# Optimization experiments

Measured on AMD Instinct MI355X. Metric: run time of the kernel, lower is better.

## Reference

```python
import jax, jax.numpy as jnp
import numpy as np
from jax import lax

D_MODEL = 1024
D_STATE = 16
D_CONV = 4
EXPAND = 2
D_INNER = EXPAND * D_MODEL  # 2048
DT_RANK = (D_MODEL + 15) // 16  # 64 (ceil(d_model/16), mamba default)
BATCH = 2
SEQLEN = 1024


def setup_inputs() -> dict:
    key = jax.random.key(0)
    ks = jax.random.split(key, 12)
    s = lambda k, shape, sc=0.02: jax.random.normal(k, shape, jnp.float32) * sc
    # A init: S4D-real, A_log = log(1..d_state) tiled over channels
    A_log = jnp.log(jnp.tile(jnp.arange(1, D_STATE + 1, dtype=jnp.float32), (D_INNER, 1)))
    # dt bias init so softplus(dt_bias) ~ 0.01
    dt_bias = jnp.log(jnp.expm1(jnp.full((D_INNER,), 0.01, jnp.float32)))
    return {
        "x": jax.random.normal(ks[0], (BATCH, SEQLEN, D_MODEL), jnp.float32),
        "in_proj_w": s(ks[1], (2 * D_INNER, D_MODEL)),
        "conv_w": s(ks[2], (D_INNER, 1, D_CONV), 0.1),
        "conv_b": s(ks[3], (D_INNER,), 0.1),
        "x_proj_w": s(ks[4], (DT_RANK + 2 * D_STATE, D_INNER)),
        "dt_proj_w": s(ks[5], (D_INNER, DT_RANK), 0.1),
        "dt_proj_b": dt_bias,
        "A_log": A_log,
        "D": jnp.ones((D_INNER,), jnp.float32),
        "out_proj_w": s(ks[6], (D_MODEL, D_INNER)),
        "ln1_g": jnp.ones((D_MODEL,), jnp.float32),
        "ln1_b": jnp.zeros((D_MODEL,), jnp.float32),
        "ln2_g": jnp.ones((D_MODEL,), jnp.float32),
        "ln2_b": jnp.zeros((D_MODEL,), jnp.float32),
        "ffn_w1": s(ks[7], (4 * D_MODEL, D_MODEL)),
        "ffn_b1": jnp.zeros((4 * D_MODEL,), jnp.float32),
        "ffn_w2": s(ks[8], (D_MODEL, 4 * D_MODEL)),
        "ffn_b2": jnp.zeros((D_MODEL,), jnp.float32),
    }


def _layernorm(x, g, b, eps=1e-5):
    mu = jnp.mean(x, axis=-1, keepdims=True)
    var = jnp.mean(jnp.square(x - mu), axis=-1, keepdims=True)
    return (x - mu) * lax.rsqrt(var + eps) * g + b


def _mamba(x, in_proj_w, conv_w, conv_b, x_proj_w, dt_proj_w, dt_proj_b,
           A_log, D, out_proj_w):
    Bsz, L, _ = x.shape
    xz = x @ in_proj_w.T                       # [B, L, 2*d_inner]
    xi, z = jnp.split(xz, 2, axis=-1)          # each [B, L, d_inner]
    # causal depthwise conv1d over time
    xc = xi.transpose(0, 2, 1)                 # [B, d_inner, L]
    xc = lax.conv_general_dilated(
        xc, conv_w, window_strides=(1,), padding=[(D_CONV - 1, 0)],
        feature_group_count=D_INNER,
        dimension_numbers=("NCH", "OIH", "NCH"))
    xc = xc + conv_b[None, :, None]
    xc = jax.nn.silu(xc).transpose(0, 2, 1)    # [B, L, d_inner]
    # input-dependent SSM params
    x_dbl = xc @ x_proj_w.T                    # [B, L, dt_rank + 2*d_state]
    dt, Bmat, Cmat = jnp.split(x_dbl, [DT_RANK, DT_RANK + D_STATE], axis=-1)
    dt = jax.nn.softplus(dt @ dt_proj_w.T + dt_proj_b)   # [B, L, d_inner]
    A = -jnp.exp(A_log)                        # [d_inner, d_state]
    dA = jnp.exp(dt[..., None] * A)                       # [B, L, d_inner, d_state]
    dBx = dt[..., None] * Bmat[:, :, None, :] * xc[..., None]  # [B, L, d_inner, d_state]
    # selective scan over time
    def step(h, inp):
        dA_t, dBx_t, C_t = inp
        h = dA_t * h + dBx_t                   # [B, d_inner, d_state]
        y = jnp.einsum("bdn,bn->bd", h, C_t)
        return h, y
    h0 = jnp.zeros((Bsz, D_INNER, D_STATE), x.dtype)
    _, ys = lax.scan(step, h0,
                     (dA.transpose(1, 0, 2, 3),
                      dBx.transpose(1, 0, 2, 3),
                      Cmat.transpose(1, 0, 2)))
    y = ys.transpose(1, 0, 2)                  # [B, L, d_inner]
    y = y + D * xc
    y = y * jax.nn.silu(z)
    return y @ out_proj_w.T                    # [B, L, d_model]


def reference(x, in_proj_w, conv_w, conv_b, x_proj_w, dt_proj_w, dt_proj_b,
              A_log, D, out_proj_w, ln1_g, ln1_b, ln2_g, ln2_b,
              ffn_w1, ffn_b1, ffn_w2, ffn_b2):
    # x = x + Mamba(LN1(x))
    x = x + _mamba(_layernorm(x, ln1_g, ln1_b), in_proj_w, conv_w, conv_b,
                   x_proj_w, dt_proj_w, dt_proj_b, A_log, D, out_proj_w)
    # x = x + FFN(LN2(x))  (dropout inactive in eval)
    h = _layernorm(x, ln2_g, ln2_b)
    f = jax.nn.relu(h @ ffn_w1.T + ffn_b1) @ ffn_w2.T + ffn_b2
    return x + f
```

## Files before the change

kernel.cpp:

```cpp
#include <hip/hip_runtime.h>
#include <hip/hip_bf16.h>

#define T_TOK 2048
#define LSEQ  1024
#define DM    1024
#define DI    2048
#define LDW2  72

using bf16 = __hip_bfloat16;
typedef __attribute__((ext_vector_type(8))) short short8;
typedef __attribute__((ext_vector_type(4))) float floatx4;

__device__ inline float to_f(float v) { return v; }
__device__ inline float to_f(bf16 v) { return __bfloat162float(v); }
__device__ inline bf16  f2bf(float v) { return __float2bfloat16(v); }
__device__ inline float bf2f(short s) { return __bfloat162float(__builtin_bit_cast(bf16, s)); }

__device__ inline short8 ld8(const bf16* p) { return *(const short8*)p; }
__device__ inline short8 ld8(const float* p) {
    floatx4 f0 = *(const floatx4*)p;
    floatx4 f1 = *(const floatx4*)(p + 4);
    short8 r;
#pragma unroll
    for (int i = 0; i < 4; ++i) {
        r[i]     = __builtin_bit_cast(short, __float2bfloat16(f0[i]));
        r[i + 4] = __builtin_bit_cast(short, __float2bfloat16(f1[i]));
    }
    return r;
}

__device__ __forceinline__ void gload16(const void* g, void* l) {
    __builtin_amdgcn_global_load_lds(
        (const __attribute__((address_space(1))) unsigned int*)g,
        (__attribute__((address_space(3))) unsigned int*)l, 16, 0, 0);
}

__device__ __forceinline__ int swz32(int row, int col) {
    return row * 32 + (col ^ (((row >> 1) & 3) << 3));
}

template<int EPI, int KS>
__device__ __forceinline__ void gemm_core(
    const bf16* __restrict__ A, int lda,
    const bf16* __restrict__ W, int K,
    float* __restrict__ outF, bf16* __restrict__ outB, int ldc,
    const float* __restrict__ bias, size_t zstr)
{
    __shared__ __align__(16) bf16 sA[128 * 32];
    __shared__ __align__(16) bf16 sW[128 * 32];
    const int tid  = threadIdx.x;
    const int lane = tid & 63, wid = tid >> 6;

    const int nwg = gridDim.x * gridDim.y * gridDim.z;
    const int lin = blockIdx.x + gridDim.x * (blockIdx.y + gridDim.y * blockIdx.z);
    const int sid = (lin & 7) * (nwg >> 3) + (lin >> 3);
    const int bx  = sid % gridDim.x;
    const int byz = sid / gridDim.x;
    const int by  = byz % gridDim.y;
    const int bz  = byz / gridDim.y;

    const int m0 = bx * 128, n0 = by * 128;
    const int wm = (wid >> 1) * 64, wn = (wid & 1) * 64;
    const int lr = lane & 15, lh = lane >> 4;

    const int r0  = tid >> 2;
    const int gc0 = ((tid & 3) * 8) ^ (((r0 >> 1) & 3) << 3);

    const int kBeg = bz * (K / KS);
    const int kEnd = kBeg + K / KS;

    const bf16* Ag0 = A + (size_t)(m0 + r0)      * lda + kBeg + gc0;
    const bf16* Ag1 = A + (size_t)(m0 + r0 + 64) * lda + kBeg + gc0;
    const bf16* Wg0 = W + (size_t)(n0 + r0)      * K   + kBeg + gc0;
    const bf16* Wg1 = W + (size_t)(n0 + r0 + 64) * K   + kBeg + gc0;

    bf16* sA0 = sA + wid * 512;
    bf16* sA1 = sA + 2048 + wid * 512;
    bf16* sW0 = sW + wid * 512;
    bf16* sW1 = sW + 2048 + wid * 512;

    floatx4 acc[4][4];
#pragma unroll
    for (int i = 0; i < 4; ++i)
#pragma unroll
        for (int j = 0; j < 4; ++j) acc[i][j] = (floatx4){0.f, 0.f, 0.f, 0.f};

    for (int k0 = kBeg; k0 < kEnd; k0 += 32) {
        __syncthreads();
        gload16(Ag0, sA0);
        gload16(Ag1, sA1);
        gload16(Wg0, sW0);
        gload16(Wg1, sW1);
        Ag0 += 32; Ag1 += 32; Wg0 += 32; Wg1 += 32;
        __syncthreads();

        short8 af[4], wf[4];
#pragma unroll
        for (int i = 0; i < 4; ++i)
            af[i] = *(const short8*)(sA + swz32(wm + i * 16 + lr, lh * 8));
#pragma unroll
        for (int j = 0; j < 4; ++j)
            wf[j] = *(const short8*)(sW + swz32(wn + j * 16 + lr, lh * 8));
#pragma unroll
        for (int i = 0; i < 4; ++i)
#pragma unroll
            for (int j = 0; j < 4; ++j)
                acc[i][j] = __builtin_amdgcn_mfma_f32_16x16x32_bf16(af[i], wf[j], acc[i][j], 0, 0, 0);
    }

#pragma unroll
    for (int i = 0; i < 4; ++i) {
#pragma unroll
        for (int j = 0; j < 4; ++j) {
#pragma unroll
            for (int r = 0; r < 4; ++r) {
                int row = m0 + wm + i * 16 + lh * 4 + r;
                int col = n0 + wn + j * 16 + lr;
                size_t off = (size_t)row * ldc + col;
                float c = acc[i][j][r];
                if (EPI == 0) {
                    outB[off] = f2bf(c);
                } else if (EPI == 2) {
                    float v = c + bias[col];
                    outB[off] = f2bf((v > 15.f) ? v : log1pf(__expf(v)));
                } else if (EPI == 4) {
                    float v = c + bias[col];
                    outB[off] = f2bf(v > 0.f ? v : 0.f);
                } else if (EPI == 7) {
                    outF[off + (size_t)bz * zstr] = c;
                } else if (EPI == 8) {
                    outB[off + (size_t)bz * zstr] = f2bf(c);
                }
            }
        }
    }
}

__launch_bounds__(256, 3)
__global__ void g_inproj(const bf16* __restrict__ A, const bf16* __restrict__ W,
                         bf16* __restrict__ outB)
{ gemm_core<0, 1>(A, DM, W, DM, nullptr, outB, 4096, nullptr, 0); }

__launch_bounds__(256, 3)
__global__ void g_xproj(const bf16* __restrict__ A, const bf16* __restrict__ W,
                        float* __restrict__ outF)
{ gemm_core<7, 16>(A, DI, W, DI, outF, nullptr, 128, nullptr, (size_t)T_TOK * 128); }

__launch_bounds__(256, 3)
__global__ void g_outproj(const bf16* __restrict__ A, const bf16* __restrict__ W,
                          bf16* __restrict__ outB)
{ gemm_core<8, 4>(A, DI, W, DI, nullptr, outB, DM, nullptr, (size_t)T_TOK * DM); }

__launch_bounds__(256, 3)
__global__ void g_ffn1(const bf16* __restrict__ A, const bf16* __restrict__ W,
                       bf16* __restrict__ outB, const float* __restrict__ bias)
{ gemm_core<4, 1>(A, DM, W, DM, nullptr, outB, 4096, bias, 0); }

__launch_bounds__(256, 3)
__global__ void g_ffn2_4(const bf16* __restrict__ A, const bf16* __restrict__ W,
                         bf16* __restrict__ outB)
{ gemm_core<8, 4>(A, 4096, W, 4096, nullptr, outB, DM, nullptr, (size_t)T_TOK * DM); }

__launch_bounds__(256, 3)
__global__ void g_ffn2_2(const bf16* __restrict__ A, const bf16* __restrict__ W,
                         bf16* __restrict__ outB)
{ gemm_core<8, 2>(A, 4096, W, 4096, nullptr, outB, DM, nullptr, (size_t)T_TOK * DM); }

__launch_bounds__(256)
__global__ void cvtw(const float* __restrict__ src, bf16* __restrict__ dst)
{
    size_t i = ((size_t)blockIdx.x * 256 + threadIdx.x) * 8;
    *(short8*)(dst + i) = ld8(src + i);
}

__launch_bounds__(256)
__global__ void cvtw4(const float* __restrict__ s0, bf16* __restrict__ d0,
                      const float* __restrict__ s1, bf16* __restrict__ d1,
                      const float* __restrict__ s2, bf16* __restrict__ d2,
                      const float* __restrict__ s3, bf16* __restrict__ d3)
{
    constexpr size_t N0 = (size_t)2 * DI * DM;
    constexpr size_t N1 = (size_t)DM * DI;
    constexpr size_t N2 = (size_t)4 * DM * DM;
    size_t i = ((size_t)blockIdx.x * 256 + threadIdx.x) * 8;
    if (i < N0) { *(short8*)(d0 + i) = ld8(s0 + i); return; }
    i -= N0;
    if (i < N1) { *(short8*)(d1 + i) = ld8(s1 + i); return; }
    i -= N1;
    if (i < N2) { *(short8*)(d2 + i) = ld8(s2 + i); return; }
    i -= N2;
    *(short8*)(d3 + i) = ld8(s3 + i);
}

__launch_bounds__(256)
__global__ void gemm_dt64(const float* __restrict__ A,
                          const float* __restrict__ W,
                          const float* __restrict__ bias,
                          bf16* __restrict__ outB)
{
    __shared__ __align__(16) bf16 sA[32 * LDW2];
    __shared__ __align__(16) bf16 sW[128 * LDW2];
    const int tid = threadIdx.x;
    const int lane = tid & 63, w = tid >> 6;
    const int m0 = blockIdx.x * 32, n0 = blockIdx.y * 128;

    {
        int ar = tid >> 3, ac = (tid & 7) * 8;
        *(short8*)(sA + ar * LDW2 + ac) = ld8(A + (size_t)(m0 + ar) * 128 + ac);
        int wr = tid >> 1, wc = (tid & 1) * 32;
        const float* wp = W + (size_t)(n0 + wr) * 64 + wc;
        *(short8*)(sW + wr * LDW2 + wc)      = ld8(wp);
        *(short8*)(sW + wr * LDW2 + wc + 8)  = ld8(wp + 8);
        *(short8*)(sW + wr * LDW2 + wc + 16) = ld8(wp + 16);
        *(short8*)(sW + wr * LDW2 + wc + 24) = ld8(wp + 24);
    }
    __syncthreads();

    const int lr = lane & 15, lh = lane >> 4;
    floatx4 acc[2][2];
#pragma unroll
    for (int i = 0; i < 2; ++i)
#pragma unroll
        for (int j = 0; j < 2; ++j) acc[i][j] = (floatx4){0.f, 0.f, 0.f, 0.f};

#pragma unroll
    for (int kk = 0; kk < 2; ++kk) {
        short8 af[2], wf[2];
#pragma unroll
        for (int i = 0; i < 2; ++i)
            af[i] = *(const short8*)(sA + (i * 16 + lr) * LDW2 + kk * 32 + lh * 8);
#pragma unroll
        for (int j = 0; j < 2; ++j)
            wf[j] = *(const short8*)(sW + (w * 32 + j * 16 + lr) * LDW2 + kk * 32 + lh * 8);
#pragma unroll
        for (int i = 0; i < 2; ++i)
#pragma unroll
            for (int j = 0; j < 2; ++j)
                acc[i][j] = __builtin_amdgcn_mfma_f32_16x16x32_bf16(af[i], wf[j], acc[i][j], 0, 0, 0);
    }

#pragma unroll
    for (int i = 0; i < 2; ++i) {
#pragma unroll
        for (int j = 0; j < 2; ++j) {
#pragma unroll
            for (int r = 0; r < 4; ++r) {
                int row = m0 + i * 16 + lh * 4 + r;
                int col = n0 + w * 32 + j * 16 + lr;
                float v = acc[i][j][r] + bias[col];
                outB[(size_t)row * DI + col] = f2bf((v > 15.f) ? v : log1pf(__expf(v)));
            }
        }
    }
}

__launch_bounds__(256)
__global__ void reduce16(const float* __restrict__ P, float* __restrict__ out)
{
    int i = blockIdx.x * 256 + threadIdx.x;
    const floatx4* P4 = (const floatx4*)P;
    floatx4 s = (floatx4){0.f, 0.f, 0.f, 0.f};
#pragma unroll
    for (int z = 0; z < 16; ++z) s += P4[(size_t)z * 65536 + i];
    ((floatx4*)out)[i] = s;
}

__launch_bounds__(256)
__global__ void red4_resid(const bf16* __restrict__ P, const float* __restrict__ x,
                           float* __restrict__ out)
{
    size_t base = ((size_t)blockIdx.x * 256 + threadIdx.x) * 8;
    floatx4 x0 = *(const floatx4*)(x + base);
    floatx4 x1 = *(const floatx4*)(x + base + 4);
    float s[8];
#pragma unroll
    for (int j = 0; j < 4; ++j) { s[j] = x0[j]; s[j + 4] = x1[j]; }
#pragma unroll
    for (int z = 0; z < 4; ++z) {
        short8 p = *(const short8*)(P + (size_t)z * T_TOK * DM + base);
#pragma unroll
        for (int j = 0; j < 8; ++j) s[j] += bf2f(p[j]);
    }
    *(floatx4*)(out + base)     = (floatx4){s[0], s[1], s[2], s[3]};
    *(floatx4*)(out + base + 4) = (floatx4){s[4], s[5], s[6], s[7]};
}

template<int Z>
__launch_bounds__(256)
__global__ void red_bias_resid(const bf16* __restrict__ P, const float* __restrict__ bias,
                               const float* __restrict__ resid, float* __restrict__ out)
{
    size_t base = ((size_t)blockIdx.x * 256 + threadIdx.x) * 8;
    int c = (int)(base & (DM - 1));
    floatx4 b0 = *(const floatx4*)(bias + c);
    floatx4 b1 = *(const floatx4*)(bias + c + 4);
    floatx4 x0 = *(const floatx4*)(resid + base);
    floatx4 x1 = *(const floatx4*)(resid + base + 4);
    float s[8];
#pragma unroll
    for (int j = 0; j < 4; ++j) { s[j] = x0[j] + b0[j]; s[j + 4] = x1[j] + b1[j]; }
#pragma unroll
    for (int z = 0; z < Z; ++z) {
        short8 p = *(const short8*)(P + (size_t)z * T_TOK * DM + base);
#pragma unroll
        for (int j = 0; j < 8; ++j) s[j] += bf2f(p[j]);
    }
    *(floatx4*)(out + base)     = (floatx4){s[0], s[1], s[2], s[3]};
    *(floatx4*)(out + base + 4) = (floatx4){s[4], s[5], s[6], s[7]};
}

__launch_bounds__(256)
__global__ void ln_kernel(const float* __restrict__ x, const float* __restrict__ g,
                          const float* __restrict__ bb, bf16* __restrict__ out)
{
    int t = blockIdx.x, tid = threadIdx.x;
    const float* xr = x + (size_t)t * DM;
    float v[4], s = 0.f, ss = 0.f;
#pragma unroll
    for (int i = 0; i < 4; ++i) {
        v[i] = xr[tid + i * 256];
        s += v[i]; ss += v[i] * v[i];
    }
#pragma unroll
    for (int o = 1; o < 64; o <<= 1) { s += __shfl_xor(s, o); ss += __shfl_xor(ss, o); }
    __shared__ float red[8];
    int lane = tid & 63, wid = tid >> 6;
    if (lane == 0) { red[wid] = s; red[wid + 4] = ss; }
    __syncthreads();
    s  = red[0] + red[1] + red[2] + red[3];
    ss = red[4] + red[5] + red[6] + red[7];
    float mu  = s * (1.f / DM);
    float var = ss * (1.f / DM) - mu * mu;
    float rs  = rsqrtf(var + 1e-5f);
#pragma unroll
    for (int i = 0; i < 4; ++i) {
        int c = tid + i * 256;
        out[(size_t)t * DM + c] = f2bf((v[i] - mu) * rs * g[c] + bb[c]);
    }
}

__launch_bounds__(256)
__global__ void conv_silu(const bf16* __restrict__ xz, const float* __restrict__ cw,
                          const float* __restrict__ cb, bf16* __restrict__ xcb)
{
    int idx = (blockIdx.x * 256 + threadIdx.x) * 8;
    int d  = idx & (DI - 1);
    int tk = idx >> 11;
    int t  = tk & (LSEQ - 1);
    const short8 zero = {0, 0, 0, 0, 0, 0, 0, 0};
    short8 x3 = ld8(xz + (size_t)tk * 4096 + d);
    short8 x2 = (t >= 1) ? ld8(xz + (size_t)(tk - 1) * 4096 + d) : zero;
    short8 x1 = (t >= 2) ? ld8(xz + (size_t)(tk - 2) * 4096 + d) : zero;
    short8 x0 = (t >= 3) ? ld8(xz + (size_t)(tk - 3) * 4096 + d) : zero;
    short8 r;
#pragma unroll
    for (int j = 0; j < 8; ++j) {
        floatx4 wv = *(const floatx4*)(cw + (size_t)(d + j) * 4);
        float acc = cb[d + j]
                  + wv[0] * bf2f(x0[j]) + wv[1] * bf2f(x1[j])
                  + wv[2] * bf2f(x2[j]) + wv[3] * bf2f(x3[j]);
        float s = acc / (1.f + __expf(-acc));
        r[j] = __builtin_bit_cast(short, f2bf(s));
    }
    *(short8*)(xcb + idx) = r;
}

__launch_bounds__(256)
__global__ void padw_kernel(const float* __restrict__ w, bf16* __restrict__ wp)
{
    int idx = blockIdx.x * 256 + threadIdx.x;
    int row = idx >> 11;
    wp[idx] = (row < 96) ? f2bf(w[idx]) : f2bf(0.f);
}

template<int NCH_>
__launch_bounds__(256)
__global__ void scan_part1(const bf16* __restrict__ dt, const bf16* __restrict__ xc,
                           const float* __restrict__ xdbl, const float* __restrict__ A_log,
                           float* __restrict__ Ssum, float* __restrict__ hend)
{
    constexpr int CLEN_ = LSEQ / NCH_;
    constexpr int LOGN  = (NCH_ == 64) ? 6 : 5;
    int G = blockIdx.x * 256 + threadIdx.x;
    int half = G & 1;
    int d = (G >> 1) & (DI - 1);
    int c = (G >> 12) & (NCH_ - 1);
    int b = G >> (12 + LOGN);
    int n0 = half * 8;

    floatx4 al0 = *(const floatx4*)(A_log + d * 16 + n0);
    floatx4 al1 = *(const floatx4*)(A_log + d * 16 + n0 + 4);
    float a[8];
#pragma unroll
    for (int j = 0; j < 4; ++j) { a[j] = -__expf(al0[j]); a[j + 4] = -__expf(al1[j]); }

    const bf16*  dt_p = dt   + (size_t)b * LSEQ * DI + d;
    const bf16*  xc_p = xc   + (size_t)b * LSEQ * DI + d;
    const float* xb_p = xdbl + (size_t)b * LSEQ * 128 + 64 + n0;

    float h[8];
#pragma unroll
    for (int j = 0; j < 8; ++j) h[j] = 0.f;
    float S = 0.f;

    const int t0 = c * CLEN_;
#pragma unroll 4
    for (int t = t0; t < t0 + CLEN_; ++t) {
        float dtv = to_f(dt_p[(size_t)t * DI]);
        float xv  = to_f(xc_p[(size_t)t * DI]);
        floatx4 B0 = *(const floatx4*)(xb_p + (size_t)t * 128);
        floatx4 B1 = *(const floatx4*)(xb_p + (size_t)t * 128 + 4);
        S += dtv;
        float dx = dtv * xv;
#pragma unroll
        for (int j = 0; j < 4; ++j) {
            h[j]     = fmaf(__expf(dtv * a[j]),     h[j],     dx * B0[j]);
            h[j + 4] = fmaf(__expf(dtv * a[j + 4]), h[j + 4], dx * B1[j]);
        }
    }

    size_t cid = (size_t)(b * NCH_ + c) * DI + d;
    if (half == 0) Ssum[cid] = S;
    float* he = hend + cid * 16 + n0;
    *(floatx4*)he       = (floatx4){h[0], h[1], h[2], h[3]};
    *(floatx4*)(he + 4) = (floatx4){h[4], h[5], h[6], h[7]};
}

template<int NCH_>
__launch_bounds__(256)
__global__ void scan_prefix(const float* __restrict__ A_log, const float* __restrict__ Ssum,
                            float* __restrict__ hend)
{
    int tid = blockIdx.x * 256 + threadIdx.x;
    int n = tid & 15;
    int d = (tid >> 4) & (DI - 1);
    int b = tid >> 15;
    float a = -__expf(A_log[d * 16 + n]);

    size_t row = (size_t)b * NCH_ * DI + d;
    float Sc = Ssum[row];
    float E  = hend[row * 16 + n];
    float h = 0.f;
    for (int c = 0; c < NCH_; ++c) {
        size_t nrow = row + DI;
        float Sn = 0.f, En = 0.f;
        if (c + 1 < NCH_) { Sn = Ssum[nrow]; En = hend[nrow * 16 + n]; }
        float P = __expf(a * Sc);
        hend[row * 16 + n] = h;
        h  = fmaf(P, h, E);
        Sc = Sn; E = En; row = nrow;
    }
}

template<int NCH_>
__launch_bounds__(256)
__global__ void scan_part2(const bf16* __restrict__ dt, const bf16* __restrict__ xc,
                           const float* __restrict__ xdbl, const bf16* __restrict__ xz,
                           const float* __restrict__ hinit, const float* __restrict__ A_log,
                           const float* __restrict__ Dp, bf16* __restrict__ Y)
{
    constexpr int CLEN_ = LSEQ / NCH_;
    constexpr int LOGN  = (NCH_ == 64) ? 6 : 5;
    int G = blockIdx.x * 256 + threadIdx.x;
    int half = G & 1;
    int d = (G >> 1) & (DI - 1);
    int c = (G >> 12) & (NCH_ - 1);
    int b = G >> (12 + LOGN);
    int n0 = half * 8;

    floatx4 al0 = *(const floatx4*)(A_log + d * 16 + n0);
    floatx4 al1 = *(const floatx4*)(A_log + d * 16 + n0 + 4);
    float a[8];
#pragma unroll
    for (int j = 0; j < 4; ++j) { a[j] = -__expf(al0[j]); a[j + 4] = -__expf(al1[j]); }
    float Dd = Dp[d];

    size_t cid = (size_t)(b * NCH_ + c) * DI + d;
    const float* hi = hinit + cid * 16 + n0;
    floatx4 h0 = *(const floatx4*)hi;
    floatx4 h1 = *(const floatx4*)(hi + 4);
    float h[8] = {h0[0], h0[1], h0[2], h0[3], h1[0], h1[1], h1[2], h1[3]};

    const bf16*  dt_p = dt   + (size_t)b * LSEQ * DI + d;
    const bf16*  xc_p = xc   + (size_t)b * LSEQ * DI + d;
    const float* xb_p = xdbl + (size_t)b * LSEQ * 128 + 64 + n0;
    const float* xcc_p= xdbl + (size_t)b * LSEQ * 128 + 80 + n0;
    const bf16*  z_p  = xz   + (size_t)b * LSEQ * 4096 + DI + d;
    bf16* y_p = Y + (size_t)b * LSEQ * DI + d;

    const int t0 = c * CLEN_;
#pragma unroll 4
    for (int t = t0; t < t0 + CLEN_; ++t) {
        float dtv = to_f(dt_p[(size_t)t * DI]);
        float xv  = to_f(xc_p[(size_t)t * DI]);
        float zv  = to_f(z_p[(size_t)t * 4096]);
        floatx4 B0 = *(const floatx4*)(xb_p  + (size_t)t * 128);
        floatx4 B1 = *(const floatx4*)(xb_p  + (size_t)t * 128 + 4);
        floatx4 C0 = *(const floatx4*)(xcc_p + (size_t)t * 128);
        floatx4 C1 = *(const floatx4*)(xcc_p + (size_t)t * 128 + 4);
        float dx = dtv * xv;
        float p = 0.f;
#pragma unroll
        for (int j = 0; j < 4; ++j) {
            h[j]     = fmaf(__expf(dtv * a[j]),     h[j],     dx * B0[j]);
            p = fmaf(h[j], C0[j], p);
            h[j + 4] = fmaf(__expf(dtv * a[j + 4]), h[j + 4], dx * B1[j]);
            p = fmaf(h[j + 4], C1[j], p);
        }
        p += __shfl_xor(p, 1);
        if (half == 0) {
            float pp = p + Dd * xv;
            float sz = zv / (1.f + __expf(-zv));
            y_p[(size_t)t * DI] = f2bf(pp * sz);
        }
    }
}

extern "C" void kernel_launch(void* const* d_in, const int* in_sizes, int n_in,
                              void* d_out, int out_size, void* d_ws, size_t ws_size,
                              hipStream_t stream)
{
    const float* x       = (const float*)d_in[0];
    const float* in_proj = (const float*)d_in[1];
    const float* conv_w  = (const float*)d_in[2];
    const float* conv_b  = (const float*)d_in[3];
    const float* x_proj  = (const float*)d_in[4];
    const float* dt_w    = (const float*)d_in[5];
    const float* dt_b    = (const float*)d_in[6];
    const float* A_log   = (const float*)d_in[7];
    const float* Dp      = (const float*)d_in[8];
    const float* out_w   = (const float*)d_in[9];
    const float* ln1g    = (const float*)d_in[10];
    const float* ln1b    = (const float*)d_in[11];
    const float* ln2g    = (const float*)d_in[12];
    const float* ln2b    = (const float*)d_in[13];
    const float* fw1     = (const float*)d_in[14];
    const float* fb1     = (const float*)d_in[15];
    const float* fw2     = (const float*)d_in[16];
    const float* fb2     = (const float*)d_in[17];
    float* out = (float*)d_out;

    char* w = (char*)d_ws;
    bf16*  h1   = (bf16*)(w);
    bf16*  xz   = (bf16*)(w + (4u  << 20));
    bf16*  xc   = (bf16*)(w + (20u << 20));
    float* xdf  = (float*)(w + (28u << 20));
    bf16*  dtb  = (bf16*)(w + (29u << 20));
    float* Pp   = (float*)(w + (29u << 20));
    float* hend = (float*)(w + (37u << 20));
    float* x2   = (float*)(w + (37u << 20));
    bf16*  Wpad = (bf16*)(w + (45u << 20));
    float* Ssum = (float*)(w);
    bf16*  Pout = (bf16*)(w + (4u  << 20));
    bf16*  Yb = xc;
    bf16*  f1 = xz;

    const bool roomy = ws_size >= ((size_t)74 << 20);

    if (roomy) {
        bf16* ipB  = (bf16*)(w + (46u << 20));
        bf16* owB  = (bf16*)(w + (54u << 20));
        bf16* fw1B = (bf16*)(w + (58u << 20));
        bf16* fw2B = (bf16*)(w + (66u << 20));
        bf16* Pf   = (bf16*)(w + (20u << 20));

        cvtw4<<<dim3(7168), dim3(256), 0, stream>>>(in_proj, ipB, out_w, owB,
                                                    fw1, fw1B, fw2, fw2B);
        ln_kernel<<<dim3(T_TOK), dim3(256), 0, stream>>>(x, ln1g, ln1b, h1);
        g_inproj<<<dim3(16, 32), dim3(256), 0, stream>>>(h1, ipB, xz);
        conv_silu<<<dim3(T_TOK * DI / 8 / 256), dim3(256), 0, stream>>>(xz, conv_w, conv_b, xc);
        padw_kernel<<<dim3(128 * 2048 / 256), dim3(256), 0, stream>>>(x_proj, Wpad);
        g_xproj<<<dim3(16, 1, 16), dim3(256), 0, stream>>>(xc, Wpad, Pp);
        reduce16<<<dim3(256), dim3(256), 0, stream>>>(Pp, xdf);
        gemm_dt64<<<dim3(64, 16), dim3(256), 0, stream>>>(xdf, dt_w, dt_b, dtb);
        scan_part1<64><<<dim3(2048), dim3(256), 0, stream>>>(dtb, xc, xdf, A_log, Ssum, hend);
        scan_prefix<64><<<dim3(256), dim3(256), 0, stream>>>(A_log, Ssum, hend);
        scan_part2<64><<<dim3(2048), dim3(256), 0, stream>>>(dtb, xc, xdf, xz, hend, A_log, Dp, Yb);
        g_outproj<<<dim3(16, 8, 4), dim3(256), 0, stream>>>(Yb, owB, Pout);
        red4_resid<<<dim3(1024), dim3(256), 0, stream>>>(Pout, x, x2);
        ln_kernel<<<dim3(T_TOK), dim3(256), 0, stream>>>(x2, ln2g, ln2b, h1);
        g_ffn1<<<dim3(16, 32), dim3(256), 0, stream>>>(h1, fw1B, f1, fb1);
        g_ffn2_4<<<dim3(16, 8, 4), dim3(256), 0, stream>>>(f1, fw2B, Pf);
        red_bias_resid<4><<<dim3(1024), dim3(256), 0, stream>>>(Pf, fb2, x2, out);
    } else {
        bf16* ipB  = (bf16*)(w + (20u << 20));
        bf16* owB  = (bf16*)(w);
        bf16* fw1B = (bf16*)(w + (29u << 20));
        bf16* fw2B = (bf16*)(w + (20u << 20));
        bf16* Pf   = (bf16*)(w + (28u << 20));

        cvtw<<<dim3(2048), dim3(256), 0, stream>>>(in_proj, ipB);
        ln_kernel<<<dim3(T_TOK), dim3(256), 0, stream>>>(x, ln1g, ln1b, h1);
        g_inproj<<<dim3(16, 32), dim3(256), 0, stream>>>(h1, ipB, xz);
        conv_silu<<<dim3(T_TOK * DI / 8 / 256), dim3(256), 0, stream>>>(xz, conv_w, conv_b, xc);
        padw_kernel<<<dim3(128 * 2048 / 256), dim3(256), 0, stream>>>(x_proj, Wpad);
        g_xproj<<<dim3(16, 1, 16), dim3(256), 0, stream>>>(xc, Wpad, Pp);
        reduce16<<<dim3(256), dim3(256), 0, stream>>>(Pp, xdf);
        gemm_dt64<<<dim3(64, 16), dim3(256), 0, stream>>>(xdf, dt_w, dt_b, dtb);
        scan_part1<32><<<dim3(1024), dim3(256), 0, stream>>>(dtb, xc, xdf, A_log, Ssum, hend);
        scan_prefix<32><<<dim3(256), dim3(256), 0, stream>>>(A_log, Ssum, hend);
        cvtw<<<dim3(1024), dim3(256), 0, stream>>>(out_w, owB);
        scan_part2<32><<<dim3(1024), dim3(256), 0, stream>>>(dtb, xc, xdf, xz, hend, A_log, Dp, Yb);
        g_outproj<<<dim3(16, 8, 4), dim3(256), 0, stream>>>(Yb, owB, Pout);
        red4_resid<<<dim3(1024), dim3(256), 0, stream>>>(Pout, x, x2);
        cvtw<<<dim3(2048), dim3(256), 0, stream>>>(fw1, fw1B);
        ln_kernel<<<dim3(T_TOK), dim3(256), 0, stream>>>(x2, ln2g, ln2b, h1);
        g_ffn1<<<dim3(16, 32), dim3(256), 0, stream>>>(h1, fw1B, f1, fb1);
        cvtw<<<dim3(2048), dim3(256), 0, stream>>>(fw2, fw2B);
        g_ffn2_2<<<dim3(16, 8, 2), dim3(256), 0, stream>>>(f1, fw2B, Pf);
        red_bias_resid<2><<<dim3(1024), dim3(256), 0, stream>>>(Pf, fb2, x2, out);
    }
}
```

Baseline: 357.7 us.

## Double-buffer GEMM LDS tiles, fuse residual reduce with LN2, fold x_proj padding into weight conversion

The shared GEMM core now keeps two LDS stages and issues the next tile's global-to-LDS loads before the MFMA work on the current tile, so memory latency overlaps compute and there is one barrier per k-step instead of two. The split-K residual reduction is merged with the second layernorm into a single per-token kernel, which removes one launch and one reread of x2. The x_proj padding is folded into the batched weight-conversion kernel, removing another launch. The costs are double the LDS per block, which may lower occupancy under launch_bounds(256,3), and an extra dummy load of a wrapped-around tile on the last iteration.

```diff
diff --git a/kernel.cpp b/kernel.cpp
--- a/kernel.cpp
+++ b/kernel.cpp
@@ -9,6 +9,7 @@
 
 using bf16 = __hip_bfloat16;
 typedef __attribute__((ext_vector_type(8))) short short8;
+typedef __attribute__((ext_vector_type(4))) short short4b;
 typedef __attribute__((ext_vector_type(4))) float floatx4;
 
 __device__ inline float to_f(float v) { return v; }
@@ -46,8 +47,8 @@
     float* __restrict__ outF, bf16* __restrict__ outB, int ldc,
     const float* __restrict__ bias, size_t zstr)
 {
-    __shared__ __align__(16) bf16 sA[128 * 32];
-    __shared__ __align__(16) bf16 sW[128 * 32];
+    __shared__ __align__(16) bf16 sA[2][128 * 32];
+    __shared__ __align__(16) bf16 sW[2][128 * 32];
     const int tid  = threadIdx.x;
     const int lane = tid & 63, wid = tid >> 6;
 
@@ -69,15 +70,10 @@
     const int kBeg = bz * (K / KS);
     const int kEnd = kBeg + K / KS;
 
-    const bf16* Ag0 = A + (size_t)(m0 + r0)      * lda + kBeg + gc0;
-    const bf16* Ag1 = A + (size_t)(m0 + r0 + 64) * lda + kBeg + gc0;
-    const bf16* Wg0 = W + (size_t)(n0 + r0)      * K   + kBeg + gc0;
-    const bf16* Wg1 = W + (size_t)(n0 + r0 + 64) * K   + kBeg + gc0;
-
-    bf16* sA0 = sA + wid * 512;
-    bf16* sA1 = sA + 2048 + wid * 512;
-    bf16* sW0 = sW + wid * 512;
-    bf16* sW1 = sW + 2048 + wid * 512;
+    const bf16* aR0 = A + (size_t)(m0 + r0)      * lda + gc0;
+    const bf16* aR1 = A + (size_t)(m0 + r0 + 64) * lda + gc0;
+    const bf16* wR0 = W + (size_t)(n0 + r0)      * K   + gc0;
+    const bf16* wR1 = W + (size_t)(n0 + r0 + 64) * K   + gc0;
 
     floatx4 acc[4][4];
 #pragma unroll
@@ -85,28 +81,51 @@
 #pragma unroll
         for (int j = 0; j < 4; ++j) acc[i][j] = (floatx4){0.f, 0.f, 0.f, 0.f};
 
-    for (int k0 = kBeg; k0 < kEnd; k0 += 32) {
-        __syncthreads();
-        gload16(Ag0, sA0);
-        gload16(Ag1, sA1);
-        gload16(Wg0, sW0);
-        gload16(Wg1, sW1);
-        Ag0 += 32; Ag1 += 32; Wg0 += 32; Wg1 += 32;
-        __syncthreads();
-
-        short8 af[4], wf[4];
-#pragma unroll
-        for (int i = 0; i < 4; ++i)
-            af[i] = *(const short8*)(sA + swz32(wm + i * 16 + lr, lh * 8));
-#pragma unroll
-        for (int j = 0; j < 4; ++j)
-            wf[j] = *(const short8*)(sW + swz32(wn + j * 16 + lr, lh * 8));
-#pragma unroll
-        for (int i = 0; i < 4; ++i)
-#pragma unroll
-            for (int j = 0; j < 4; ++j)
-                acc[i][j] = __builtin_amdgcn_mfma_f32_16x16x32_bf16(af[i], wf[j], acc[i][j], 0, 0, 0);
-    }
+#define STAGE(B, KK) do {                                       \
+        gload16(aR0 + (KK), &sA[B][wid * 512]);                 \
+        gload16(aR1 + (KK), &sA[B][2048 + wid * 512]);          \
+        gload16(wR0 + (KK), &sW[B][wid * 512]);                 \
+        gload16(wR1 + (KK), &sW[B][2048 + wid * 512]);          \
+    } while (0)
+
+#define COMPUTE(B) do {                                                        \
+        short8 af[4], wf[4];                                                   \
+        _Pragma("unroll")                                                      \
+        for (int i = 0; i < 4; ++i)                                            \
+            af[i] = *(const short8*)(&sA[B][swz32(wm + i * 16 + lr, lh * 8)]); \
+        _Pragma("unroll")                                                      \
+        for (int j = 0; j < 4; ++j)                                            \
+            wf[j] = *(const short8*)(&sW[B][swz32(wn + j * 16 + lr, lh * 8)]); \
+        _Pragma("unroll")                                                      \
+        for (int i = 0; i < 4; ++i)                                            \
+            _Pragma("unroll")                                                  \
+            for (int j = 0; j < 4; ++j)                                        \
+                acc[i][j] = __builtin_amdgcn_mfma_f32_16x16x32_bf16(           \
+                    af[i], wf[j], acc[i][j], 0, 0, 0);                         \
+    } while (0)
+
+#define PHASE_SYNC() do {                                       \
+        __builtin_amdgcn_sched_barrier(0);                      \
+        asm volatile("s_waitcnt vmcnt(0)" ::: "memory");        \
+        __builtin_amdgcn_s_barrier();                           \
+        __builtin_amdgcn_sched_barrier(0);                      \
+    } while (0)
+
+    STAGE(0, kBeg);
+    PHASE_SYNC();
+
+    for (int k0 = kBeg; k0 < kEnd; k0 += 64) {
+        STAGE(1, k0 + 32);
+        COMPUTE(0);
+        PHASE_SYNC();
+        int kn = (k0 + 64 < kEnd) ? k0 + 64 : kBeg;
+        STAGE(0, kn);
+        COMPUTE(1);
+        PHASE_SYNC();
+    }
+#undef STAGE
+#undef COMPUTE
+#undef PHASE_SYNC
 
 #pragma unroll
     for (int i = 0; i < 4; ++i) {
@@ -174,14 +193,16 @@
 }
 
 __launch_bounds__(256)
-__global__ void cvtw4(const float* __restrict__ s0, bf16* __restrict__ d0,
+__global__ void cvtw5(const float* __restrict__ s0, bf16* __restrict__ d0,
                       const float* __restrict__ s1, bf16* __restrict__ d1,
                       const float* __restrict__ s2, bf16* __restrict__ d2,
-                      const float* __restrict__ s3, bf16* __restrict__ d3)
+                      const float* __restrict__ s3, bf16* __restrict__ d3,
+                      const float* __restrict__ s4, bf16* __restrict__ d4)
 {
     constexpr size_t N0 = (size_t)2 * DI * DM;
     constexpr size_t N1 = (size_t)DM * DI;
     constexpr size_t N2 = (size_t)4 * DM * DM;
+    constexpr size_t N3 = (size_t)DM * 4 * DM;
     size_t i = ((size_t)blockIdx.x * 256 + threadIdx.x) * 8;
     if (i < N0) { *(short8*)(d0 + i) = ld8(s0 + i); return; }
     i -= N0;
@@ -189,7 +210,11 @@
     i -= N1;
     if (i < N2) { *(short8*)(d2 + i) = ld8(s2 + i); return; }
     i -= N2;
-    *(short8*)(d3 + i) = ld8(s3 + i);
+    if (i < N3) { *(short8*)(d3 + i) = ld8(s3 + i); return; }
+    i -= N3;
+    int row = (int)(i >> 11);
+    if (row < 96) { *(short8*)(d4 + i) = ld8(s4 + i); }
+    else { *(short8*)(d4 + i) = (short8){0,0,0,0,0,0,0,0}; }
 }
 
 __launch_bounds__(256)
@@ -266,23 +291,42 @@
 }
 
 __launch_bounds__(256)
-__global__ void red4_resid(const bf16* __restrict__ P, const float* __restrict__ x,
-                           float* __restrict__ out)
-{
-    size_t base = ((size_t)blockIdx.x * 256 + threadIdx.x) * 8;
-    floatx4 x0 = *(const floatx4*)(x + base);
-    floatx4 x1 = *(const floatx4*)(x + base + 4);
-    float s[8];
-#pragma unroll
-    for (int j = 0; j < 4; ++j) { s[j] = x0[j]; s[j + 4] = x1[j]; }
+__global__ void red4_ln(const bf16* __restrict__ P, const float* __restrict__ x,
+                        const float* __restrict__ g, const float* __restrict__ bb,
+                        float* __restrict__ x2, bf16* __restrict__ h1)
+{
+    int t = blockIdx.x, tid = threadIdx.x;
+    size_t rowoff = (size_t)t * DM + tid * 4;
+    floatx4 xv = *(const floatx4*)(x + rowoff);
+    float v[4];
+#pragma unroll
+    for (int i = 0; i < 4; ++i) v[i] = xv[i];
 #pragma unroll
     for (int z = 0; z < 4; ++z) {
-        short8 p = *(const short8*)(P + (size_t)z * T_TOK * DM + base);
-#pragma unroll
-        for (int j = 0; j < 8; ++j) s[j] += bf2f(p[j]);
-    }
-    *(floatx4*)(out + base)     = (floatx4){s[0], s[1], s[2], s[3]};
-    *(floatx4*)(out + base + 4) = (floatx4){s[4], s[5], s[6], s[7]};
+        short4b p = *(const short4b*)(P + (size_t)z * T_TOK * DM + rowoff);
+#pragma unroll
+        for (int i = 0; i < 4; ++i) v[i] += bf2f(p[i]);
+    }
+    *(floatx4*)(x2 + rowoff) = (floatx4){v[0], v[1], v[2], v[3]};
+    float s = v[0] + v[1] + v[2] + v[3];
+    float ss = v[0]*v[0] + v[1]*v[1] + v[2]*v[2] + v[3]*v[3];
+#pragma unroll
+    for (int o = 1; o < 64; o <<= 1) { s += __shfl_xor(s, o); ss += __shfl_xor(ss, o); }
+    __shared__ float red[8];
+    int lane = tid & 63, wid = tid >> 6;
+    if (lane == 0) { red[wid] = s; red[wid + 4] = ss; }
+    __syncthreads();
+    s  = red[0] + red[1] + red[2] + red[3];
+    ss = red[4] + red[5] + red[6] + red[7];
+    float mu  = s * (1.f / DM);
+    float var = ss * (1.f / DM) - mu * mu;
+    float rs  = rsqrtf(var + 1e-5f);
+    int c = tid * 4;
+    short4b o4;
+#pragma unroll
+    for (int i = 0; i < 4; ++i)
+        o4[i] = __builtin_bit_cast(short, f2bf((v[i] - mu) * rs * g[c + i] + bb[c + i]));
+    *(short4b*)(h1 + rowoff) = o4;
 }
 
 template<int Z>
@@ -564,12 +608,11 @@
         bf16* fw2B = (bf16*)(w + (66u << 20));
         bf16* Pf   = (bf16*)(w + (20u << 20));
 
-        cvtw4<<<dim3(7168), dim3(256), 0, stream>>>(in_proj, ipB, out_w, owB,
-                                                    fw1, fw1B, fw2, fw2B);
+        cvtw5<<<dim3(7296), dim3(256), 0, stream>>>(in_proj, ipB, out_w, owB,
+                                                    fw1, fw1B, fw2, fw2B, x_proj, Wpad);
         ln_kernel<<<dim3(T_TOK), dim3(256), 0, stream>>>(x, ln1g, ln1b, h1);
         g_inproj<<<dim3(16, 32), dim3(256), 0, stream>>>(h1, ipB, xz);
         conv_silu<<<dim3(T_TOK * DI / 8 / 256), dim3(256), 0, stream>>>(xz, conv_w, conv_b, xc);
-        padw_kernel<<<dim3(128 * 2048 / 256), dim3(256), 0, stream>>>(x_proj, Wpad);
         g_xproj<<<dim3(16, 1, 16), dim3(256), 0, stream>>>(xc, Wpad, Pp);
         reduce16<<<dim3(256), dim3(256), 0, stream>>>(Pp, xdf);
         gemm_dt64<<<dim3(64, 16), dim3(256), 0, stream>>>(xdf, dt_w, dt_b, dtb);
@@ -577,8 +620,7 @@
         scan_prefix<64><<<dim3(256), dim3(256), 0, stream>>>(A_log, Ssum, hend);
         scan_part2<64><<<dim3(2048), dim3(256), 0, stream>>>(dtb, xc, xdf, xz, hend, A_log, Dp, Yb);
         g_outproj<<<dim3(16, 8, 4), dim3(256), 0, stream>>>(Yb, owB, Pout);
-        red4_resid<<<dim3(1024), dim3(256), 0, stream>>>(Pout, x, x2);
-        ln_kernel<<<dim3(T_TOK), dim3(256), 0, stream>>>(x2, ln2g, ln2b, h1);
+        red4_ln<<<dim3(T_TOK), dim3(256), 0, stream>>>(Pout, x, ln2g, ln2b, x2, h1);
         g_ffn1<<<dim3(16, 32), dim3(256), 0, stream>>>(h1, fw1B, f1, fb1);
         g_ffn2_4<<<dim3(16, 8, 4), dim3(256), 0, stream>>>(f1, fw2B, Pf);
         red_bias_resid<4><<<dim3(1024), dim3(256), 0, stream>>>(Pf, fb2, x2, out);
@@ -602,9 +644,8 @@
         cvtw<<<dim3(1024), dim3(256), 0, stream>>>(out_w, owB);
         scan_part2<32><<<dim3(1024), dim3(256), 0, stream>>>(dtb, xc, xdf, xz, hend, A_log, Dp, Yb);
         g_outproj<<<dim3(16, 8, 4), dim3(256), 0, stream>>>(Yb, owB, Pout);
-        red4_resid<<<dim3(1024), dim3(256), 0, stream>>>(Pout, x, x2);
         cvtw<<<dim3(2048), dim3(256), 0, stream>>>(fw1, fw1B);
-        ln_kernel<<<dim3(T_TOK), dim3(256), 0, stream>>>(x2, ln2g, ln2b, h1);
+        red4_ln<<<dim3(T_TOK), dim3(256), 0, stream>>>(Pout, x, ln2g, ln2b, x2, h1);
         g_ffn1<<<dim3(16, 32), dim3(256), 0, stream>>>(h1, fw1B, f1, fb1);
         cvtw<<<dim3(2048), dim3(256), 0, stream>>>(fw2, fw2B);
         g_ffn2_2<<<dim3(16, 8, 2), dim3(256), 0, stream>>>(f1, fw2B, Pf);
```

New measurement: 377.2 us. +5.5%, slower.
